# Optimization experiments

Measured on AMD Instinct MI355X. Metric: run time of the kernel, lower is better.

The kernel has to match this reference:

```python
import jax, jax.numpy as jnp
import numpy as np

V_MAX = 3.0
FEATURE_CLAMP = 10.0
TOP_K = 1


def _green_diag(d):
    """Diagonal of G = (tridiag(sub=1, diag=d, super=1))^{-1} for each batch row.
    d: (B, N) complex64. Stable two-sided continued-fraction (Thomas-like) recurrences:
      L_i = d_i - 1/L_{i-1},  U_i = d_i - 1/U_{i+1},  G_ii = 1/(L_i + U_i - d_i).
    Sequential over N (vectorized over B) via lax.scan.
    """
    dT = d.T  # (N, B)

    def step(c, di):
        nc = di - 1.0 / c
        return nc, nc

    L0 = dT[0]
    _, Lr = jax.lax.scan(step, L0, dT[1:])
    L = jnp.concatenate([L0[None], Lr], axis=0)  # (N, B)

    dR = dT[::-1]
    U0 = dR[0]
    _, Ur = jax.lax.scan(step, U0, dR[1:])
    U = jnp.concatenate([U0[None], Ur], axis=0)[::-1]  # (N, B)

    return (1.0 / (L + U - dT)).T  # (B, N)


def setup_inputs() -> dict:
    key = jax.random.key(0)
    B, N, D, E, F = 4, 4096, 512, 4, 2048
    ks = jax.random.split(key, 8)
    s = lambda k, sh, sc: (jax.random.normal(k, sh, jnp.float32) * sc)
    return dict(
        x=jax.random.normal(ks[0], (B, N, D), jnp.float32),
        v_proj_w=s(ks[1], (1, D), D ** -0.5),
        v_proj_b=jnp.zeros((1,), jnp.float32),
        gamma=jnp.float32(0.0),
        epsilon_param=jnp.float32(1.0),
        gate_w=s(ks[2], (E, D), D ** -0.5),
        gate_b=jnp.zeros((E,), jnp.float32),
        w1=s(ks[3], (E, D, F), D ** -0.5),
        b1=jnp.zeros((E, F), jnp.float32),
        w2=s(ks[4], (E, F, D), F ** -0.5),
        b2=jnp.zeros((E, D), jnp.float32),
        out_w=s(ks[5], (D, 2), 0.5),
        out_b=jnp.zeros((D,), jnp.float32),
        bk_scale=jnp.ones((D,), jnp.float32),
    )


def reference(x, v_proj_w, v_proj_b, gamma, epsilon_param, gate_w, gate_b,
              w1, b1, w2, b2, out_w, out_b, bk_scale):
    # 1) scalar potential from tokens
    v = jnp.einsum('bnd,od->bno', x, v_proj_w)[..., 0] + v_proj_b[0]  # (B, N)
    v = jnp.clip(v, -V_MAX, V_MAX)

    # 2) gamma-shifted complex tridiagonal Green's function diagonal
    eps = jax.nn.softplus(epsilon_param) + 1e-6
    z = 1j * (eps + gamma)                       # complex64 scalar
    d = ((v - 2.0).astype(jnp.complex64) - z)    # he_diag - z, (B, N)
    G = _green_diag(d)                            # (B, N) complex
    feats = jnp.clip(jnp.stack([G.real, G.imag], axis=-1), -FEATURE_CLAMP, FEATURE_CLAMP)  # (B,N,2)

    # 3) sparse MoE FFN (top-1 routing, experts = Linear -> GELU -> Linear)
    logits = jnp.einsum('bnd,ed->bne', x, gate_w) + gate_b
    probs = jax.nn.softmax(logits, axis=-1)
    top_p, top_i = jax.lax.top_k(probs, TOP_K)
    top_w = top_p / jnp.sum(top_p, axis=-1, keepdims=True)
    wmask = jnp.sum(jax.nn.one_hot(top_i, probs.shape[-1], dtype=probs.dtype) * top_w[..., None], axis=-2)  # (B,N,E)

    h = jax.nn.gelu(jnp.einsum('bnd,edf->benf', x, w1) + b1[None, :, None, :], approximate=False)
    y = jnp.einsum('benf,efd->bend', h, w2) + b2[None, :, None, :]
    ffn_out = jnp.einsum('bne,bend->bnd', wmask, y)

    # 4) combine spectral features with FFN output
    spec_out = jnp.einsum('bnc,dc->bnd', feats, out_w) + out_b
    return ffn_out + bk_scale * spec_out
```

## Files before the change

kernel.cpp:

```cpp
#include <hip/hip_runtime.h>
#include <hip/hip_bf16.h>
#include <math.h>


typedef __bf16 bf16x8 __attribute__((ext_vector_type(8)));
typedef float  f32x4  __attribute__((ext_vector_type(4)));
typedef __attribute__((address_space(3))) __bf16 lbf16;

#define B_   4
#define N_   4096
#define D_   512
#define E_   4
#define F_   2048
#define T_   (B_*N_)
#define CAP_ T_
#define R256 68
#define PADROWS (R256*256)

#define LGKM_BARRIER() asm volatile("s_waitcnt lgkmcnt(0)\n\ts_barrier" ::: "memory")

__device__ __forceinline__ void gload_lds16(const __bf16* g, lbf16* l) {
    __builtin_amdgcn_global_load_lds(
        (__attribute__((address_space(1))) void*)(void*)g,
        (__attribute__((address_space(3))) void*)l, 16, 0, 0);
}

__device__ __forceinline__ float fast_gelu(float x) {
    float u = 1.5957691216f * fmaf(0.044715f * x, x * x, x);
    return x / (1.0f + __expf(-u));
}

__device__ __forceinline__ void load8f2(const float2* p, float2* dst) {
    const float4* q = (const float4*)p;
    #pragma unroll
    for (int i = 0; i < 4; ++i) {
        float4 t = q[i];
        dst[2*i]   = make_float2(t.x, t.y);
        dst[2*i+1] = make_float2(t.z, t.w);
    }
}

__device__ __forceinline__ void mfma_tile(const char* Ab, const char* Bb,
                                          int cs0, int cs1, f32x4 acc[4][4]) {
    #pragma unroll
    for (int ks = 0; ks < 2; ++ks) {
        int cs = ks ? cs1 : cs0;
        bf16x8 af[4], bfr[4];
        #pragma unroll
        for (int m = 0; m < 4; ++m)
            af[m] = *(const bf16x8*)(Ab + m * 2048 + cs);
        #pragma unroll
        for (int n = 0; n < 4; ++n)
            bfr[n] = *(const bf16x8*)(Bb + n * 2048 + cs);
        #pragma unroll
        for (int m = 0; m < 4; ++m)
            #pragma unroll
            for (int n = 0; n < 4; ++n)
                acc[m][n] = __builtin_amdgcn_mfma_f32_16x16x32_bf16(af[m], bfr[n], acc[m][n], 0, 0, 0);
    }
}

__device__ alignas(256) __bf16 s_w1t[(size_t)E_*F_*D_];
__device__ alignas(256) __bf16 s_w2t[(size_t)E_*D_*F_];
__device__ alignas(256) __bf16 s_xb[(size_t)PADROWS*D_];
__device__ alignas(256) __bf16 s_H[(size_t)PADROWS*F_];
__device__ alignas(256) float2 s_d[T_];
__device__ alignas(256) float2 s_feats[T_];
__device__ alignas(256) float2 s_L[T_];
__device__ alignas(256) float2 s_U[T_];
__device__ alignas(256) int    s_perm[E_*CAP_];
__device__ alignas(256) int    s_cnt[E_];
__device__ alignas(256) int    s_tpre[8];
__device__ alignas(256) int    s_eid[T_];

__global__ void transpose_both_kernel(const float* __restrict__ w1,
                                      const float* __restrict__ w2,
                                      __bf16* __restrict__ w1t,
                                      __bf16* __restrict__ w2t) {
    __shared__ alignas(16) float tile[32][33];
    int idx = blockIdx.x;
    int which = idx >> 12;
    int r = idx & 4095;
    int e = r >> 10;
    int t = r & 1023;
    int R, C, c0, r0;
    const float* s;
    __bf16* d;
    if (which == 0) { R = D_; C = F_; c0 = (t & 63) * 32; r0 = (t >> 6) * 32;
                      s = w1 + (size_t)e * R * C; d = w1t + (size_t)e * R * C; }
    else            { R = F_; C = D_; c0 = (t & 15) * 32; r0 = (t >> 4) * 32;
                      s = w2 + (size_t)e * R * C; d = w2t + (size_t)e * R * C; }
    int tx = threadIdx.x, ty = threadIdx.y;
    #pragma unroll
    for (int i = 0; i < 4; ++i)
        tile[ty + i*8][tx] = s[(size_t)(r0 + ty + i*8) * C + c0 + tx];
    __syncthreads();
    #pragma unroll
    for (int i = 0; i < 4; ++i)
        d[(size_t)(c0 + ty + i*8) * R + r0 + tx] = (__bf16)tile[tx][ty + i*8];
}

__device__ inline float dot8(float4 a, float4 b, float4 c, float4 d) {
    float s =      a.x * c.x;
    s = fmaf(a.y, c.y, s); s = fmaf(a.z, c.z, s); s = fmaf(a.w, c.w, s);
    s = fmaf(b.x, d.x, s); s = fmaf(b.y, d.y, s); s = fmaf(b.z, d.z, s);
    s = fmaf(b.w, d.w, s);
    return s;
}

__device__ inline float wave_sum(float s) {
    #pragma unroll
    for (int off = 32; off > 0; off >>= 1) s += __shfl_xor(s, off);
    return s;
}

__global__ __launch_bounds__(256) void prep_kernel(
        const float* __restrict__ x,
        const float* __restrict__ vw, const float* __restrict__ vb,
        const float* __restrict__ gamma, const float* __restrict__ epsp,
        const float* __restrict__ gw, const float* __restrict__ gb,
        float2* __restrict__ dbuf, int* __restrict__ eid) {
    int wv = threadIdx.x >> 6, lane = threadIdx.x & 63;
    int token = blockIdx.x * 4 + wv;
    const float4* xr = (const float4*)(x + (size_t)token * D_);
    float4 xa = xr[lane*2], xb = xr[lane*2 + 1];

    const float4* vr = (const float4*)vw;
    float sv = dot8(xa, xb, vr[lane*2], vr[lane*2 + 1]);
    float sg0, sg1, sg2, sg3;
    {
        const float4* g0 = (const float4*)(gw + 0*D_);
        const float4* g1 = (const float4*)(gw + 1*D_);
        const float4* g2 = (const float4*)(gw + 2*D_);
        const float4* g3 = (const float4*)(gw + 3*D_);
        sg0 = dot8(xa, xb, g0[lane*2], g0[lane*2+1]);
        sg1 = dot8(xa, xb, g1[lane*2], g1[lane*2+1]);
        sg2 = dot8(xa, xb, g2[lane*2], g2[lane*2+1]);
        sg3 = dot8(xa, xb, g3[lane*2], g3[lane*2+1]);
    }
    sv  = wave_sum(sv);
    sg0 = wave_sum(sg0); sg1 = wave_sum(sg1);
    sg2 = wave_sum(sg2); sg3 = wave_sum(sg3);

    if (lane == 0) {
        float v = sv + vb[0];
        v = fminf(fmaxf(v, -3.0f), 3.0f);
        float eps = log1pf(expf(epsp[0])) + 1e-6f;
        dbuf[token] = make_float2(v - 2.0f, -(eps + gamma[0]));

        float l0 = sg0 + gb[0], l1 = sg1 + gb[1], l2 = sg2 + gb[2], l3 = sg3 + gb[3];
        float best = l0; int be = 0;
        if (l1 > best) { best = l1; be = 1; }
        if (l2 > best) { best = l2; be = 2; }
        if (l3 > best) { best = l3; be = 3; }
        eid[token] = be;
    }
}

__global__ __launch_bounds__(1024) void route_scan_kernel(
        const int* __restrict__ eid, int* __restrict__ perm,
        int* __restrict__ cnt, int* __restrict__ tpre,
        const float2* __restrict__ dbuf, float2* __restrict__ Lb,
        float2* __restrict__ Ub, float2* __restrict__ feats) {
    int tid = threadIdx.x;
    if (blockIdx.x == 0) {
        __shared__ int chunkcnt[256][4];
        __shared__ int chunkoff[256][4];
        __shared__ int totals[4];
        int wv = tid >> 6, lane = tid & 63;

        for (int c = wv; c < 256; c += 16) {
            int e = eid[c * 64 + lane];
            unsigned long long m0 = __ballot(e == 0);
            unsigned long long m1 = __ballot(e == 1);
            unsigned long long m2 = __ballot(e == 2);
            unsigned long long m3 = __ballot(e == 3);
            if (lane == 0) {
                chunkcnt[c][0] = __popcll(m0);
                chunkcnt[c][1] = __popcll(m1);
                chunkcnt[c][2] = __popcll(m2);
                chunkcnt[c][3] = __popcll(m3);
            }
        }
        __syncthreads();

        if (wv < 4) {
            int e = wv, carry = 0;
            #pragma unroll
            for (int g = 0; g < 4; ++g) {
                int idx = g * 64 + lane;
                int v = chunkcnt[idx][e];
                int s = v;
                #pragma unroll
                for (int off = 1; off < 64; off <<= 1) {
                    int u = __shfl_up(s, off);
                    if (lane >= off) s += u;
                }
                chunkoff[idx][e] = carry + s - v;
                carry += __shfl(s, 63);
            }
            if (lane == 0) { cnt[e] = carry; totals[e] = carry; }
        }
        __syncthreads();
        if (tid == 0) {
            int acc = 0;
            #pragma unroll
            for (int e = 0; e < E_; ++e) { tpre[e] = acc; acc += (totals[e] + 255) >> 8; }
            tpre[4] = acc;
        }

        for (int c = wv; c < 256; c += 16) {
            int t = c * 64 + lane;
            int e = eid[t];
            unsigned long long m0 = __ballot(e == 0);
            unsigned long long m1 = __ballot(e == 1);
            unsigned long long m2 = __ballot(e == 2);
            unsigned long long m3 = __ballot(e == 3);
            unsigned long long mym = (e == 0) ? m0 : (e == 1) ? m1 : (e == 2) ? m2 : m3;
            unsigned long long below = lane ? (mym & ((1ull << lane) - 1ull)) : 0ull;
            int pos = chunkoff[c][e] + __popcll(below);
            perm[e * CAP_ + pos] = t;
        }
    } else {
        __shared__ alignas(16) float chunkM[8][64][8];
        __shared__ alignas(16) float bound[8][64][4];
        int s = tid >> 6, c = tid & 63;
        int b = s & 3, dir = (s >> 2) & 1;

        if (tid < 512) {
            float ar=1, ai=0, br=0, bi=0, cr=0, ci=0, dr=1, di=0;
            float2 cur[8], nxt[8];
            {
                int seq0 = c * 64;
                const float2* p = dbuf + (dir ? (b*N_ + N_ - 8 - seq0) : (b*N_ + seq0));
                load8f2(p, cur);
            }
            for (int g = 0; g < 8; ++g) {
                if (g < 7) {
                    int seq0 = c * 64 + (g + 1) * 8;
                    const float2* p = dbuf + (dir ? (b*N_ + N_ - 8 - seq0) : (b*N_ + seq0));
                    load8f2(p, nxt);
                }
                #pragma unroll
                for (int q = 0; q < 8; ++q) {
                    float2 dv = dir ? cur[7 - q] : cur[q];
                    float nar = dv.x*ar - dv.y*ai - cr;
                    float nai = dv.x*ai + dv.y*ar - ci;
                    float nbr = dv.x*br - dv.y*bi - dr;
                    float nbi = dv.x*bi + dv.y*br - di;
                    cr = ar; ci = ai; dr = br; di = bi;
                    ar = nar; ai = nai; br = nbr; bi = nbi;
                }
                float m = fmaxf(fmaxf(fmaxf(fabsf(ar),fabsf(ai)),fmaxf(fabsf(br),fabsf(bi))),
                                fmaxf(fmaxf(fabsf(cr),fabsf(ci)),fmaxf(fabsf(dr),fabsf(di))));
                float inv = 1.0f / fmaxf(m, 1e-30f);
                ar*=inv; ai*=inv; br*=inv; bi*=inv; cr*=inv; ci*=inv; dr*=inv; di*=inv;
                #pragma unroll
                for (int q = 0; q < 8; ++q) cur[q] = nxt[q];
            }
            float* cm = chunkM[s][c];
            cm[0]=ar; cm[1]=ai; cm[2]=br; cm[3]=bi; cm[4]=cr; cm[5]=ci; cm[6]=dr; cm[7]=di;
        }
        __syncthreads();

        if (tid < 8) {
            int ss = tid;
            float pr=1, pi=0, qr=0, qi=0;
            for (int cc = 0; cc < 64; ++cc) {
                float* bd = bound[ss][cc];
                bd[0]=pr; bd[1]=pi; bd[2]=qr; bd[3]=qi;
                const float* m = chunkM[ss][cc];
                float npr = m[0]*pr - m[1]*pi + m[2]*qr - m[3]*qi;
                float npi = m[0]*pi + m[1]*pr + m[2]*qi + m[3]*qr;
                float nqr = m[4]*pr - m[5]*pi + m[6]*qr - m[7]*qi;
                float nqi = m[4]*pi + m[5]*pr + m[6]*qi + m[7]*qr;
                float mx = fmaxf(fmaxf(fabsf(npr),fabsf(npi)), fmaxf(fabsf(nqr),fabsf(nqi)));
                float inv = 1.0f / fmaxf(mx, 1e-30f);
                pr = npr*inv; pi = npi*inv; qr = nqr*inv; qi = nqi*inv;
            }
        }
        __syncthreads();

        if (tid < 512) {
            const float* bd = bound[s][c];
            float pr=bd[0], pi=bd[1], qr=bd[2], qi=bd[3];
            float den = fmaxf(pr*pr + pi*pi, 1e-30f);
            float invr = (qr*pr + qi*pi) / den;
            float invi = (qi*pr - qr*pi) / den;
            float2 cur[8], nxt[8];
            {
                int seq0 = c * 64;
                const float2* p = dbuf + (dir ? (b*N_ + N_ - 8 - seq0) : (b*N_ + seq0));
                load8f2(p, cur);
            }
            for (int g = 0; g < 8; ++g) {
                if (g < 7) {
                    int seq0 = c * 64 + (g + 1) * 8;
                    const float2* p = dbuf + (dir ? (b*N_ + N_ - 8 - seq0) : (b*N_ + seq0));
                    load8f2(p, nxt);
                }
                #pragma unroll
                for (int q = 0; q < 8; ++q) {
                    int seq = c * 64 + g * 8 + q;
                    int orig = dir ? (N_ - 1 - seq) : seq;
                    int t = b * N_ + orig;
                    float2 dv = dir ? cur[7 - q] : cur[q];
                    float Lr = dv.x - invr, Li = dv.y - invi;
                    if (dir) Ub[t] = make_float2(Lr, Li);
                    else     Lb[t] = make_float2(Lr, Li);
                    float d2 = Lr*Lr + Li*Li;
                    invr = Lr / d2; invi = -Li / d2;
                }
                #pragma unroll
                for (int q = 0; q < 8; ++q) cur[q] = nxt[q];
            }
        }
        __threadfence();
        __syncthreads();

        for (int t = tid; t < T_; t += 1024) {
            float2 L = Lb[t], U = Ub[t], dv = dbuf[t];
            float sr = L.x + U.x - dv.x;
            float si = L.y + U.y - dv.y;
            float den = sr*sr + si*si;
            float Gr = sr / den, Gi = -si / den;
            Gr = fminf(fmaxf(Gr, -10.0f), 10.0f);
            Gi = fminf(fmaxf(Gi, -10.0f), 10.0f);
            feats[t] = make_float2(Gr, Gi);
        }
    }
}

__global__ __launch_bounds__(256) void reorder_kernel(
        const float* __restrict__ x, const int* __restrict__ perm,
        const int* __restrict__ cnt, const int* __restrict__ tpre,
        __bf16* __restrict__ xb) {
    int wv = threadIdx.x >> 6, lane = threadIdx.x & 63;
    int prow = blockIdx.x * 4 + wv;
    if (prow >= tpre[4] * 256) return;
    int e = 0;
    #pragma unroll
    for (int k = 1; k < E_; ++k) if (prow >= tpre[k] * 256) e = k;
    int i = prow - tpre[e] * 256;
    int token = (i < cnt[e]) ? perm[e * CAP_ + i] : -1;
    bf16x8 v = {0,0,0,0,0,0,0,0};
    if (token >= 0) {
        const float4* xr = (const float4*)(x + (size_t)token * D_);
        float4 a = xr[lane*2], b = xr[lane*2 + 1];
        v = (bf16x8){(__bf16)a.x,(__bf16)a.y,(__bf16)a.z,(__bf16)a.w,
                     (__bf16)b.x,(__bf16)b.y,(__bf16)b.z,(__bf16)b.w};
    }
    *(bf16x8*)(xb + (size_t)prow * D_ + lane * 8) = v;
}

__global__ __launch_bounds__(512, 4) void gemm1_kernel(
        const __bf16* __restrict__ xb, const __bf16* __restrict__ w1t,
        const float* __restrict__ b1, __bf16* __restrict__ Hb,
        const int* __restrict__ tpre) {
    int bid = blockIdx.x;
    int lb  = (bid & 7) * 136 + (bid >> 3);
    int rt = lb >> 4, ct = lb & 15;
    if (rt >= tpre[4]) return;
    int e = 0;
    #pragma unroll
    for (int k = 1; k < E_; ++k) if (rt >= tpre[k]) e = k;

    __shared__ __bf16 A[256 * 64];
    __shared__ __bf16 Bm[128 * 64];

    int tid = threadIdx.x, lane = tid & 63, wv = tid >> 6;
    int fl = lane & 15, gl = lane >> 4;
    int wr = wv >> 1, wc = wv & 1;

    int r8    = lane >> 3;
    int scolb = ((lane & 7) * 16) ^ (r8 << 4);
    const __bf16* aS0 = xb  + (size_t)(rt * 256 + wv * 32 + r8) * 512 + (scolb >> 1);
    const __bf16* bS0 = w1t + (size_t)(e * F_ + ct * 128 + wv * 16 + r8) * 512 + (scolb >> 1);
    lbf16* aD0 = (lbf16*)A  + wv * 32 * 64;
    lbf16* bD0 = (lbf16*)Bm + wv * 16 * 64;

    int xorv = (fl & 7) << 4;
    int cs0 = (gl * 16) ^ xorv;
    int cs1 = (64 + gl * 16) ^ xorv;
    const char* Ab = (const char*)A  + (wr * 64 + fl) * 128;
    const char* Bb = (const char*)Bm + (wc * 64 + fl) * 128;

    f32x4 acc[4][4];
    #pragma unroll
    for (int m = 0; m < 4; ++m)
        #pragma unroll
        for (int n = 0; n < 4; ++n) acc[m][n] = (f32x4){0.f,0.f,0.f,0.f};

    #pragma unroll
    for (int i = 0; i < 4; ++i)
        gload_lds16(aS0 + (size_t)i * 8 * 512, aD0 + i * 512);
    #pragma unroll
    for (int i = 0; i < 2; ++i)
        gload_lds16(bS0 + (size_t)i * 8 * 512, bD0 + i * 512);

    for (int kt = 0; kt < 8; ++kt) {
        __syncthreads();
        mfma_tile(Ab, Bb, cs0, cs1, acc);
        if (kt + 1 < 8) {
            LGKM_BARRIER();
            #pragma unroll
            for (int i = 0; i < 4; ++i)
                gload_lds16(aS0 + (size_t)i * 8 * 512 + (kt + 1) * 64, aD0 + i * 512);
            #pragma unroll
            for (int i = 0; i < 2; ++i)
                gload_lds16(bS0 + (size_t)i * 8 * 512 + (kt + 1) * 64, bD0 + i * 512);
        }
    }

    int gre = rt * 256 + wr * 64;
    int gce = ct * 128 + wc * 64;
    float b1v[4];
    #pragma unroll
    for (int n = 0; n < 4; ++n) b1v[n] = b1[e * F_ + gce + n*16 + fl];
    #pragma unroll
    for (int m = 0; m < 4; ++m)
        #pragma unroll
        for (int r = 0; r < 4; ++r) {
            __bf16* hrow = Hb + (size_t)(gre + m*16 + gl*4 + r) * F_ + gce;
            #pragma unroll
            for (int n = 0; n < 4; ++n)
                hrow[n*16 + fl] = (__bf16)fast_gelu(acc[m][n][r] + b1v[n]);
        }
}

__global__ __launch_bounds__(512, 4) void gemm2_kernel(
        const __bf16* __restrict__ Hb, const __bf16* __restrict__ w2t,
        const float* __restrict__ b2, const float* __restrict__ outw,
        const float* __restrict__ outb, const float* __restrict__ bk,
        const float2* __restrict__ feats, const int* __restrict__ perm,
        const int* __restrict__ cnt_p, const int* __restrict__ tpre,
        float* __restrict__ out) {
    int bid = blockIdx.x;
    int lb  = (bid & 7) * 34 + (bid >> 3);
    int rt = lb >> 2, ct = lb & 3;
    if (rt >= tpre[4]) return;
    int e = 0;
    #pragma unroll
    for (int k = 1; k < E_; ++k) if (rt >= tpre[k]) e = k;

    __shared__ __bf16 A[256 * 64];
    __shared__ __bf16 Bm[128 * 64];

    int tid = threadIdx.x, lane = tid & 63, wv = tid >> 6;
    int fl = lane & 15, gl = lane >> 4;
    int wr = wv >> 1, wc = wv & 1;

    int r8    = lane >> 3;
    int scolb = ((lane & 7) * 16) ^ (r8 << 4);
    const __bf16* aS0 = Hb  + (size_t)(rt * 256 + wv * 32 + r8) * F_ + (scolb >> 1);
    const __bf16* bS0 = w2t + (size_t)(e * D_ + ct * 128 + wv * 16 + r8) * F_ + (scolb >> 1);
    lbf16* aD0 = (lbf16*)A  + wv * 32 * 64;
    lbf16* bD0 = (lbf16*)Bm + wv * 16 * 64;

    int xorv = (fl & 7) << 4;
    int cs0 = (gl * 16) ^ xorv;
    int cs1 = (64 + gl * 16) ^ xorv;
    const char* Ab = (const char*)A  + (wr * 64 + fl) * 128;
    const char* Bb = (const char*)Bm + (wc * 64 + fl) * 128;

    f32x4 acc[4][4];
    #pragma unroll
    for (int m = 0; m < 4; ++m)
        #pragma unroll
        for (int n = 0; n < 4; ++n) acc[m][n] = (f32x4){0.f,0.f,0.f,0.f};

    #pragma unroll
    for (int i = 0; i < 4; ++i)
        gload_lds16(aS0 + (size_t)i * 8 * F_, aD0 + i * 512);
    #pragma unroll
    for (int i = 0; i < 2; ++i)
        gload_lds16(bS0 + (size_t)i * 8 * F_, bD0 + i * 512);

    for (int kt = 0; kt < 32; ++kt) {
        __syncthreads();
        mfma_tile(Ab, Bb, cs0, cs1, acc);
        if (kt + 1 < 32) {
            LGKM_BARRIER();
            #pragma unroll
            for (int i = 0; i < 4; ++i)
                gload_lds16(aS0 + (size_t)i * 8 * F_ + (kt + 1) * 64, aD0 + i * 512);
            #pragma unroll
            for (int i = 0; i < 2; ++i)
                gload_lds16(bS0 + (size_t)i * 8 * F_ + (kt + 1) * 64, bD0 + i * 512);
        }
    }

    int cnt = cnt_p[e];
    int ibase = rt * 256 + wr * 64 - tpre[e] * 256;
    int gce = ct * 128 + wc * 64;
    float c_b2[4], c_o0[4], c_o1[4], c_ob[4], c_bk[4];
    #pragma unroll
    for (int n = 0; n < 4; ++n) {
        int dcol = gce + n*16 + fl;
        c_b2[n] = b2[e * D_ + dcol];
        c_o0[n] = outw[dcol * 2 + 0];
        c_o1[n] = outw[dcol * 2 + 1];
        c_ob[n] = outb[dcol];
        c_bk[n] = bk[dcol];
    }
    #pragma unroll
    for (int m = 0; m < 4; ++m)
        #pragma unroll
        for (int r = 0; r < 4; ++r) {
            int i = ibase + m*16 + gl*4 + r;
            if (i >= cnt) continue;
            int token = perm[e * CAP_ + i];
            float2 ft = feats[token];
            float* orow = out + (size_t)token * D_;
            #pragma unroll
            for (int n = 0; n < 4; ++n) {
                int dcol = gce + n*16 + fl;
                float spec = ft.x * c_o0[n] + ft.y * c_o1[n] + c_ob[n];
                orow[dcol] = acc[m][n][r] + c_b2[n] + c_bk[n] * spec;
            }
        }
}

extern "C" void kernel_launch(void* const* d_in, const int* in_sizes, int n_in,
                              void* d_out, int out_size, void* d_ws, size_t ws_size,
                              hipStream_t stream) {
    const float* x     = (const float*)d_in[0];
    const float* vpw   = (const float*)d_in[1];
    const float* vpb   = (const float*)d_in[2];
    const float* gamma = (const float*)d_in[3];
    const float* epsp  = (const float*)d_in[4];
    const float* gw    = (const float*)d_in[5];
    const float* gb    = (const float*)d_in[6];
    const float* w1    = (const float*)d_in[7];
    const float* b1    = (const float*)d_in[8];
    const float* w2    = (const float*)d_in[9];
    const float* b2    = (const float*)d_in[10];
    const float* ow    = (const float*)d_in[11];
    const float* ob    = (const float*)d_in[12];
    const float* bk    = (const float*)d_in[13];
    float* out = (float*)d_out;

    const size_t szW  = (size_t)E_ * F_ * D_ * sizeof(__bf16);
    const size_t szF2 = (size_t)T_ * sizeof(float2);
    const size_t szPm = (size_t)E_ * CAP_ * sizeof(int);
    const size_t szCt = 256;
    const size_t szXb = (size_t)PADROWS * D_ * sizeof(__bf16);
    const size_t szH  = (size_t)PADROWS * F_ * sizeof(__bf16);
    const size_t szEi = (size_t)T_ * sizeof(int);
    size_t need = 2*szW + 4*szF2 + szPm + 2*szCt + szXb + szH + szEi + 16*256;

    __bf16 *w1t, *w2t, *xbuf, *Hbuf; float2 *dbuf, *Lb, *Ub, *feats;
    int *perm, *cnt, *tpre, *eid;
    int use_ws = (d_ws != nullptr && ws_size >= need);
    if (use_ws) {
        size_t off = 0;
        auto carve = [&](size_t bytes) {
            void* p = (char*)d_ws + off;
            off += (bytes + 255) & ~(size_t)255;
            return p;
        };
        w1t   = (__bf16*)carve(szW);
        w2t   = (__bf16*)carve(szW);
        xbuf  = (__bf16*)carve(szXb);
        Hbuf  = (__bf16*)carve(szH);
        dbuf  = (float2*)carve(szF2);
        Lb    = (float2*)carve(szF2);
        Ub    = (float2*)carve(szF2);
        feats = (float2*)carve(szF2);
        perm  = (int*)   carve(szPm);
        cnt   = (int*)   carve(szCt);
        tpre  = (int*)   carve(szCt);
        eid   = (int*)   carve(szEi);
    } else {
        void* p;
        hipGetSymbolAddress(&p, HIP_SYMBOL(s_w1t));  w1t   = (__bf16*)p;
        hipGetSymbolAddress(&p, HIP_SYMBOL(s_w2t));  w2t   = (__bf16*)p;
        hipGetSymbolAddress(&p, HIP_SYMBOL(s_xb));   xbuf  = (__bf16*)p;
        hipGetSymbolAddress(&p, HIP_SYMBOL(s_H));    Hbuf  = (__bf16*)p;
        hipGetSymbolAddress(&p, HIP_SYMBOL(s_d));    dbuf  = (float2*)p;
        hipGetSymbolAddress(&p, HIP_SYMBOL(s_L));    Lb    = (float2*)p;
        hipGetSymbolAddress(&p, HIP_SYMBOL(s_U));    Ub    = (float2*)p;
        hipGetSymbolAddress(&p, HIP_SYMBOL(s_feats));feats = (float2*)p;
        hipGetSymbolAddress(&p, HIP_SYMBOL(s_perm)); perm  = (int*)p;
        hipGetSymbolAddress(&p, HIP_SYMBOL(s_cnt));  cnt   = (int*)p;
        hipGetSymbolAddress(&p, HIP_SYMBOL(s_tpre)); tpre  = (int*)p;
        hipGetSymbolAddress(&p, HIP_SYMBOL(s_eid));  eid   = (int*)p;
    }

    dim3 tb(32, 8);
    transpose_both_kernel<<<8192, tb, 0, stream>>>(w1, w2, w1t, w2t);
    prep_kernel<<<T_/4, 256, 0, stream>>>(x, vpw, vpb, gamma, epsp, gw, gb, dbuf, eid);
    route_scan_kernel<<<2, 1024, 0, stream>>>(eid, perm, cnt, tpre, dbuf, Lb, Ub, feats);
    reorder_kernel<<<PADROWS/4, 256, 0, stream>>>(x, perm, cnt, tpre, xbuf);
    gemm1_kernel<<<R256*16, 512, 0, stream>>>(xbuf, w1t, b1, Hbuf, tpre);
    gemm2_kernel<<<R256*4, 512, 0, stream>>>(Hbuf, w2t, b2, ow, ob, bk,
                                             feats, perm, cnt, tpre, out);
}
```

Before: 201.0 us.

## Fuse weight transpose into prep kernel and double-buffer A tile in gemm1

```diff
diff --git a/kernel.cpp b/kernel.cpp
--- a/kernel.cpp
+++ b/kernel.cpp
@@ -73,33 +73,6 @@
 __device__ alignas(256) int    s_tpre[8];
 __device__ alignas(256) int    s_eid[T_];
 
-__global__ void transpose_both_kernel(const float* __restrict__ w1,
-                                      const float* __restrict__ w2,
-                                      __bf16* __restrict__ w1t,
-                                      __bf16* __restrict__ w2t) {
-    __shared__ alignas(16) float tile[32][33];
-    int idx = blockIdx.x;
-    int which = idx >> 12;
-    int r = idx & 4095;
-    int e = r >> 10;
-    int t = r & 1023;
-    int R, C, c0, r0;
-    const float* s;
-    __bf16* d;
-    if (which == 0) { R = D_; C = F_; c0 = (t & 63) * 32; r0 = (t >> 6) * 32;
-                      s = w1 + (size_t)e * R * C; d = w1t + (size_t)e * R * C; }
-    else            { R = F_; C = D_; c0 = (t & 15) * 32; r0 = (t >> 4) * 32;
-                      s = w2 + (size_t)e * R * C; d = w2t + (size_t)e * R * C; }
-    int tx = threadIdx.x, ty = threadIdx.y;
-    #pragma unroll
-    for (int i = 0; i < 4; ++i)
-        tile[ty + i*8][tx] = s[(size_t)(r0 + ty + i*8) * C + c0 + tx];
-    __syncthreads();
-    #pragma unroll
-    for (int i = 0; i < 4; ++i)
-        d[(size_t)(c0 + ty + i*8) * R + r0 + tx] = (__bf16)tile[tx][ty + i*8];
-}
-
 __device__ inline float dot8(float4 a, float4 b, float4 c, float4 d) {
     float s =      a.x * c.x;
     s = fmaf(a.y, c.y, s); s = fmaf(a.z, c.z, s); s = fmaf(a.w, c.w, s);
@@ -114,46 +87,73 @@
     return s;
 }
 
-__global__ __launch_bounds__(256) void prep_kernel(
+__global__ __launch_bounds__(256) void prep_trans_kernel(
+        const float* __restrict__ w1, const float* __restrict__ w2,
+        __bf16* __restrict__ w1t, __bf16* __restrict__ w2t,
         const float* __restrict__ x,
         const float* __restrict__ vw, const float* __restrict__ vb,
         const float* __restrict__ gamma, const float* __restrict__ epsp,
         const float* __restrict__ gw, const float* __restrict__ gb,
         float2* __restrict__ dbuf, int* __restrict__ eid) {
-    int wv = threadIdx.x >> 6, lane = threadIdx.x & 63;
-    int token = blockIdx.x * 4 + wv;
-    const float4* xr = (const float4*)(x + (size_t)token * D_);
-    float4 xa = xr[lane*2], xb = xr[lane*2 + 1];
-
-    const float4* vr = (const float4*)vw;
-    float sv = dot8(xa, xb, vr[lane*2], vr[lane*2 + 1]);
-    float sg0, sg1, sg2, sg3;
-    {
-        const float4* g0 = (const float4*)(gw + 0*D_);
-        const float4* g1 = (const float4*)(gw + 1*D_);
-        const float4* g2 = (const float4*)(gw + 2*D_);
-        const float4* g3 = (const float4*)(gw + 3*D_);
-        sg0 = dot8(xa, xb, g0[lane*2], g0[lane*2+1]);
-        sg1 = dot8(xa, xb, g1[lane*2], g1[lane*2+1]);
-        sg2 = dot8(xa, xb, g2[lane*2], g2[lane*2+1]);
-        sg3 = dot8(xa, xb, g3[lane*2], g3[lane*2+1]);
-    }
-    sv  = wave_sum(sv);
-    sg0 = wave_sum(sg0); sg1 = wave_sum(sg1);
-    sg2 = wave_sum(sg2); sg3 = wave_sum(sg3);
-
-    if (lane == 0) {
-        float v = sv + vb[0];
-        v = fminf(fmaxf(v, -3.0f), 3.0f);
-        float eps = log1pf(expf(epsp[0])) + 1e-6f;
-        dbuf[token] = make_float2(v - 2.0f, -(eps + gamma[0]));
-
-        float l0 = sg0 + gb[0], l1 = sg1 + gb[1], l2 = sg2 + gb[2], l3 = sg3 + gb[3];
-        float best = l0; int be = 0;
-        if (l1 > best) { best = l1; be = 1; }
-        if (l2 > best) { best = l2; be = 2; }
-        if (l3 > best) { best = l3; be = 3; }
-        eid[token] = be;
+    __shared__ alignas(16) float tile[32][33];
+    int idx = blockIdx.x;
+    int tid = threadIdx.x;
+    if (idx < 8192) {
+        int which = idx >> 12;
+        int r = idx & 4095;
+        int e = r >> 10;
+        int t = r & 1023;
+        int R, C, c0, r0;
+        const float* s;
+        __bf16* d;
+        if (which == 0) { R = D_; C = F_; c0 = (t & 63) * 32; r0 = (t >> 6) * 32;
+                          s = w1 + (size_t)e * R * C; d = w1t + (size_t)e * R * C; }
+        else            { R = F_; C = D_; c0 = (t & 15) * 32; r0 = (t >> 4) * 32;
+                          s = w2 + (size_t)e * R * C; d = w2t + (size_t)e * R * C; }
+        int tx = tid & 31, ty = tid >> 5;
+        #pragma unroll
+        for (int i = 0; i < 4; ++i)
+            tile[ty + i*8][tx] = s[(size_t)(r0 + ty + i*8) * C + c0 + tx];
+        __syncthreads();
+        #pragma unroll
+        for (int i = 0; i < 4; ++i)
+            d[(size_t)(c0 + ty + i*8) * R + r0 + tx] = (__bf16)tile[tx][ty + i*8];
+    } else {
+        int wv = tid >> 6, lane = tid & 63;
+        int token = (idx - 8192) * 4 + wv;
+        const float4* xr = (const float4*)(x + (size_t)token * D_);
+        float4 xa = xr[lane*2], xb = xr[lane*2 + 1];
+
+        const float4* vr = (const float4*)vw;
+        float sv = dot8(xa, xb, vr[lane*2], vr[lane*2 + 1]);
+        float sg0, sg1, sg2, sg3;
+        {
+            const float4* g0 = (const float4*)(gw + 0*D_);
+            const float4* g1 = (const float4*)(gw + 1*D_);
+            const float4* g2 = (const float4*)(gw + 2*D_);
+            const float4* g3 = (const float4*)(gw + 3*D_);
+            sg0 = dot8(xa, xb, g0[lane*2], g0[lane*2+1]);
+            sg1 = dot8(xa, xb, g1[lane*2], g1[lane*2+1]);
+            sg2 = dot8(xa, xb, g2[lane*2], g2[lane*2+1]);
+            sg3 = dot8(xa, xb, g3[lane*2], g3[lane*2+1]);
+        }
+        sv  = wave_sum(sv);
+        sg0 = wave_sum(sg0); sg1 = wave_sum(sg1);
+        sg2 = wave_sum(sg2); sg3 = wave_sum(sg3);
+
+        if (lane == 0) {
+            float v = sv + vb[0];
+            v = fminf(fmaxf(v, -3.0f), 3.0f);
+            float eps = log1pf(expf(epsp[0])) + 1e-6f;
+            dbuf[token] = make_float2(v - 2.0f, -(eps + gamma[0]));
+
+            float l0 = sg0 + gb[0], l1 = sg1 + gb[1], l2 = sg2 + gb[2], l3 = sg3 + gb[3];
+            float best = l0; int be = 0;
+            if (l1 > best) { best = l1; be = 1; }
+            if (l2 > best) { best = l2; be = 2; }
+            if (l3 > best) { best = l3; be = 3; }
+            eid[token] = be;
+        }
     }
 }
 
@@ -353,7 +353,7 @@
     *(bf16x8*)(xb + (size_t)prow * D_ + lane * 8) = v;
 }
 
-__global__ __launch_bounds__(512, 4) void gemm1_kernel(
+__global__ __launch_bounds__(512, 2) void gemm1_kernel(
         const __bf16* __restrict__ xb, const __bf16* __restrict__ w1t,
         const float* __restrict__ b1, __bf16* __restrict__ Hb,
         const int* __restrict__ tpre) {
@@ -365,8 +365,9 @@
     #pragma unroll
     for (int k = 1; k < E_; ++k) if (rt >= tpre[k]) e = k;
 
-    __shared__ __bf16 A[256 * 64];
-    __shared__ __bf16 Bm[128 * 64];
+    extern __shared__ char smem[];
+    char* Abase = smem;
+    char* Bbase = smem + 65536;
 
     int tid = threadIdx.x, lane = tid & 63, wv = tid >> 6;
     int fl = lane & 15, gl = lane >> 4;
@@ -376,14 +377,16 @@
     int scolb = ((lane & 7) * 16) ^ (r8 << 4);
     const __bf16* aS0 = xb  + (size_t)(rt * 256 + wv * 32 + r8) * 512 + (scolb >> 1);
     const __bf16* bS0 = w1t + (size_t)(e * F_ + ct * 128 + wv * 16 + r8) * 512 + (scolb >> 1);
-    lbf16* aD0 = (lbf16*)A  + wv * 32 * 64;
-    lbf16* bD0 = (lbf16*)Bm + wv * 16 * 64;
+    lbf16* aD[2] = { (lbf16*)Abase + wv * 2048,
+                     (lbf16*)(Abase + 32768) + wv * 2048 };
+    lbf16* bD0   = (lbf16*)Bbase + wv * 1024;
 
     int xorv = (fl & 7) << 4;
     int cs0 = (gl * 16) ^ xorv;
     int cs1 = (64 + gl * 16) ^ xorv;
-    const char* Ab = (const char*)A  + (wr * 64 + fl) * 128;
-    const char* Bb = (const char*)Bm + (wc * 64 + fl) * 128;
+    const char* Ab[2] = { Abase + (wr * 64 + fl) * 128,
+                          Abase + 32768 + (wr * 64 + fl) * 128 };
+    const char* Bb = Bbase + (wc * 64 + fl) * 128;
 
     f32x4 acc[4][4];
     #pragma unroll
@@ -393,19 +396,22 @@
 
     #pragma unroll
     for (int i = 0; i < 4; ++i)
-        gload_lds16(aS0 + (size_t)i * 8 * 512, aD0 + i * 512);
+        gload_lds16(aS0 + (size_t)i * 8 * 512, aD[0] + i * 512);
     #pragma unroll
     for (int i = 0; i < 2; ++i)
         gload_lds16(bS0 + (size_t)i * 8 * 512, bD0 + i * 512);
 
     for (int kt = 0; kt < 8; ++kt) {
         __syncthreads();
-        mfma_tile(Ab, Bb, cs0, cs1, acc);
+        int cur = kt & 1;
+        if (kt + 1 < 8) {
+            #pragma unroll
+            for (int i = 0; i < 4; ++i)
+                gload_lds16(aS0 + (size_t)i * 8 * 512 + (kt + 1) * 64, aD[cur ^ 1] + i * 512);
+        }
+        mfma_tile(Ab[cur], Bb, cs0, cs1, acc);
         if (kt + 1 < 8) {
             LGKM_BARRIER();
-            #pragma unroll
-            for (int i = 0; i < 4; ++i)
-                gload_lds16(aS0 + (size_t)i * 8 * 512 + (kt + 1) * 64, aD0 + i * 512);
             #pragma unroll
             for (int i = 0; i < 2; ++i)
                 gload_lds16(bS0 + (size_t)i * 8 * 512 + (kt + 1) * 64, bD0 + i * 512);
@@ -587,12 +593,19 @@
         hipGetSymbolAddress(&p, HIP_SYMBOL(s_eid));  eid   = (int*)p;
     }
 
-    dim3 tb(32, 8);
-    transpose_both_kernel<<<8192, tb, 0, stream>>>(w1, w2, w1t, w2t);
-    prep_kernel<<<T_/4, 256, 0, stream>>>(x, vpw, vpb, gamma, epsp, gw, gb, dbuf, eid);
+    static int lds_attr_set = 0;
+    if (!lds_attr_set) {
+        hipFuncSetAttribute((const void*)gemm1_kernel,
+                            hipFuncAttributeMaxDynamicSharedMemorySize, 81920);
+        lds_attr_set = 1;
+    }
+
+    prep_trans_kernel<<<12288, 256, 0, stream>>>(w1, w2, w1t, w2t,
+                                                 x, vpw, vpb, gamma, epsp, gw, gb,
+                                                 dbuf, eid);
     route_scan_kernel<<<2, 1024, 0, stream>>>(eid, perm, cnt, tpre, dbuf, Lb, Ub, feats);
     reorder_kernel<<<PADROWS/4, 256, 0, stream>>>(x, perm, cnt, tpre, xbuf);
-    gemm1_kernel<<<R256*16, 512, 0, stream>>>(xbuf, w1t, b1, Hbuf, tpre);
+    gemm1_kernel<<<R256*16, 512, 81920, stream>>>(xbuf, w1t, b1, Hbuf, tpre);
     gemm2_kernel<<<R256*4, 512, 0, stream>>>(Hbuf, w2t, b2, ow, ob, bk,
                                              feats, perm, cnt, tpre, out);
 }
```

Result: slower. 215.4 us (+7.2%).
